# Kernel tuning notes

Hardware: AMD Instinct MI355X
Metric: run time of the kernel (lower is better)

Reference implementation:

```python
import jax, jax.numpy as jnp
import numpy as np

DIM = 1024
HEADS = 16
DIM_HEAD = 64
INNER = HEADS * DIM_HEAD  # 1024


def setup_inputs() -> dict:
    key = jax.random.key(0)
    k1, k2, k3, k4 = jax.random.split(key, 4)
    x = jax.random.normal(k1, (4, 2048, DIM), dtype=jnp.float32)
    # nn.Linear(dim, 3*inner, bias=False): weight (3*inner, dim); store transposed (dim, 3*inner)
    w_qkv = jax.random.normal(k2, (DIM, 3 * INNER), dtype=jnp.float32) * (DIM ** -0.5)
    # nn.Linear(inner, dim) with bias
    w_out = jax.random.normal(k3, (INNER, DIM), dtype=jnp.float32) * (INNER ** -0.5)
    b_out = jax.random.normal(k4, (DIM,), dtype=jnp.float32) * 0.01
    return {"x": x, "w_qkv": w_qkv, "w_out": w_out, "b_out": b_out}


def reference(x, w_qkv, w_out, b_out):
    b, n, _ = x.shape
    scale = DIM_HEAD ** -0.5
    qkv = x @ w_qkv  # [b, n, 3*inner]
    q, k, v = jnp.split(qkv, 3, axis=-1)
    # 'b n (h d) -> b h n d'
    def split_heads(t):
        return t.reshape(b, n, HEADS, DIM_HEAD).transpose(0, 2, 1, 3)
    q, k, v = split_heads(q), split_heads(k), split_heads(v)
    sim = jnp.einsum('bhid,bhjd->bhij', q, k) * scale  # [b, h, n, n]
    attn = jax.nn.softmax(sim, axis=-1)
    out = jnp.einsum('bhij,bhjd->bhid', attn, v)  # [b, h, n, d]
    out = out.transpose(0, 2, 1, 3).reshape(b, n, INNER)  # 'b h n d -> b n (h d)'
    return out @ w_out + b_out
```

## Files before the change

### kernel.cpp

```cpp
#include <hip/hip_runtime.h>
#include <hip/hip_bf16.h>

#define BATCH 4
#define SEQ   2048
#define DIM   1024
#define HEADS 16
#define DHEAD 64
#define INNER 1024
#define QKV_N 3072
#define MTOT  8192

typedef short bf16x8 __attribute__((ext_vector_type(8)));
typedef float f32x4  __attribute__((ext_vector_type(4)));
#define MFMA16(a,b,c) __builtin_amdgcn_mfma_f32_16x16x32_bf16((a),(b),(c),0,0,0)

#define QSCALE 0.1803368801111204f

static __device__ __forceinline__ unsigned fau(float f) { return __float_as_uint(f); }

static __device__ __forceinline__ uint2 pack_hi4(float4 v) {
    return make_uint2((fau(v.x) >> 16) | (fau(v.y) & 0xffff0000u),
                      (fau(v.z) >> 16) | (fau(v.w) & 0xffff0000u));
}
static __device__ __forceinline__ float4 resid4(float4 v) {
    float4 r;
    r.x = v.x - __uint_as_float(fau(v.x) & 0xffff0000u);
    r.y = v.y - __uint_as_float(fau(v.y) & 0xffff0000u);
    r.z = v.z - __uint_as_float(fau(v.z) & 0xffff0000u);
    r.w = v.w - __uint_as_float(fau(v.w) & 0xffff0000u);
    return r;
}
static __device__ __forceinline__ uint2 pack_lo4(float4 v) { return pack_hi4(resid4(v)); }

static __device__ __forceinline__ unsigned cvt_pk_bf16(float a, float b) {
    unsigned r;
    asm("v_cvt_pk_bf16_f32 %0, %1, %2" : "=v"(r) : "v"(a), "v"(b));
    return r;
}

__global__ __launch_bounds__(256) void pack_rows_hl(const float* __restrict__ src,
                                                    unsigned short* __restrict__ dst,
                                                    int Mtot, int K)
{
    const int m = blockIdx.x * 256 + threadIdx.x;
    const int t = blockIdx.y;
    const float* sp = src + (size_t)m * K + t * 32;
    unsigned short buf[64];
    #pragma unroll
    for (int i = 0; i < 32; i += 4) {
        const float4 v = *(const float4*)&sp[i];
        *(uint2*)&buf[i]      = pack_hi4(v);
        *(uint2*)&buf[32 + i] = pack_lo4(v);
    }
    unsigned short* dp = dst + ((size_t)t * Mtot + m) * 64;
    const int s7 = m & 7;
    #pragma unroll
    for (int G = 0; G < 8; ++G)
        *(bf16x8*)&dp[(G ^ s7) * 8] = *(bf16x8*)&buf[G * 8];
}

__global__ __launch_bounds__(256) void pack_cols_hl(const float* __restrict__ src,
                                                    unsigned short* __restrict__ dst,
                                                    int Ntot)
{
    const int n = blockIdx.x * 256 + threadIdx.x;
    const int t = blockIdx.y;
    float vals[32];
    #pragma unroll
    for (int i = 0; i < 32; ++i) vals[i] = src[(size_t)(t * 32 + i) * Ntot + n];
    unsigned short buf[64];
    #pragma unroll
    for (int i = 0; i < 32; i += 4) {
        const float4 v = make_float4(vals[i], vals[i + 1], vals[i + 2], vals[i + 3]);
        *(uint2*)&buf[i]      = pack_hi4(v);
        *(uint2*)&buf[32 + i] = pack_lo4(v);
    }
    unsigned short* dp = dst + ((size_t)t * Ntot + n) * 64;
    const int s7 = n & 7;
    #pragma unroll
    for (int G = 0; G < 8; ++G)
        *(bf16x8*)&dp[(G ^ s7) * 8] = *(bf16x8*)&buf[G * 8];
}

static __device__ __forceinline__ void gemm_core_pk(const unsigned short* __restrict__ Ap,
                                                    const unsigned short* __restrict__ Bp,
                                                    unsigned short* As,
                                                    unsigned short* Bs,
                                                    f32x4 (&acc)[4][4],
                                                    int Mtot, int Ntot, int NT,
                                                    int row0, int col0)
{
    const int tid  = threadIdx.x;
    const int lane = tid & 63;
    const int w    = tid >> 6;
    const int l15  = lane & 15;
    const int g    = lane >> 4;
    const int wr   = w >> 1, wc = w & 1;

    const unsigned short* aSrc = Ap + (size_t)row0 * 64 + tid * 8;
    const unsigned short* bSrc = Bp + (size_t)col0 * 64 + tid * 8;
    const size_t aStep = (size_t)Mtot * 64;
    const size_t bStep = (size_t)Ntot * 64;

    int aoff[4][2], boff[4][2];
    #pragma unroll
    for (int mt = 0; mt < 4; ++mt) {
        const int m = wr * 64 + mt * 16 + l15;
        const int sw = (m & 7) << 3;
        aoff[mt][0] = m * 64 + ((g * 8) ^ sw);
        aoff[mt][1] = m * 64 + ((32 + g * 8) ^ sw);
    }
    #pragma unroll
    for (int nt = 0; nt < 4; ++nt) {
        const int n = wc * 64 + nt * 16 + l15;
        const int sw = (n & 7) << 3;
        boff[nt][0] = n * 64 + ((g * 8) ^ sw);
        boff[nt][1] = n * 64 + ((32 + g * 8) ^ sw);
    }

    bf16x8 ar[4], br[4];
    #pragma unroll
    for (int p = 0; p < 4; ++p) {
        ar[p] = *(const bf16x8*)(aSrc + p * 2048);
        br[p] = *(const bf16x8*)(bSrc + p * 2048);
    }

    for (int t = 0; t < NT; ++t) {
        __syncthreads();
        #pragma unroll
        for (int p = 0; p < 4; ++p) {
            *(bf16x8*)&As[tid * 8 + p * 2048] = ar[p];
            *(bf16x8*)&Bs[tid * 8 + p * 2048] = br[p];
        }
        __syncthreads();
        if (t + 1 < NT) {
            const unsigned short* a2 = aSrc + (size_t)(t + 1) * aStep;
            const unsigned short* b2 = bSrc + (size_t)(t + 1) * bStep;
            #pragma unroll
            for (int p = 0; p < 4; ++p) {
                ar[p] = *(const bf16x8*)(a2 + p * 2048);
                br[p] = *(const bf16x8*)(b2 + p * 2048);
            }
        }
        bf16x8 ah[4], al[4], bh[4], bl[4];
        #pragma unroll
        for (int mt = 0; mt < 4; ++mt) {
            ah[mt] = *(const bf16x8*)&As[aoff[mt][0]];
            al[mt] = *(const bf16x8*)&As[aoff[mt][1]];
        }
        #pragma unroll
        for (int nt = 0; nt < 4; ++nt) {
            bh[nt] = *(const bf16x8*)&Bs[boff[nt][0]];
            bl[nt] = *(const bf16x8*)&Bs[boff[nt][1]];
        }
        #pragma unroll
        for (int mt = 0; mt < 4; ++mt)
            #pragma unroll
            for (int nt = 0; nt < 4; ++nt) {
                acc[mt][nt] = MFMA16(ah[mt], bh[nt], acc[mt][nt]);
                acc[mt][nt] = MFMA16(ah[mt], bl[nt], acc[mt][nt]);
                acc[mt][nt] = MFMA16(al[mt], bh[nt], acc[mt][nt]);
            }
    }
}

__global__ __launch_bounds__(256, 2) void gemm_out_pk(const unsigned short* __restrict__ Ap,
                                                      const unsigned short* __restrict__ Bp,
                                                      const float* __restrict__ bias,
                                                      float* __restrict__ C)
{
    __shared__ unsigned short As[128 * 64];
    __shared__ unsigned short Bs[128 * 64];

    const int tid  = threadIdx.x;
    const int lane = tid & 63;
    const int w    = tid >> 6;
    const int l15  = lane & 15;
    const int g    = lane >> 4;
    const int wr   = w >> 1, wc = w & 1;
    const int row0 = blockIdx.y * 128, col0 = blockIdx.x * 128;

    f32x4 acc[4][4] = {};
    gemm_core_pk(Ap, Bp, As, Bs, acc, MTOT, INNER, 32, row0, col0);

    #pragma unroll
    for (int nt = 0; nt < 4; ++nt) {
        const int c = col0 + wc * 64 + nt * 16 + l15;
        const float bv = bias[c];
        #pragma unroll
        for (int mt = 0; mt < 4; ++mt)
            #pragma unroll
            for (int r = 0; r < 4; ++r) {
                const int rr = row0 + wr * 64 + mt * 16 + g * 4 + r;
                C[(size_t)rr * INNER + c] = acc[mt][nt][r] + bv;
            }
    }
}

__global__ __launch_bounds__(256, 2) void gemm_qkv_pk(const unsigned short* __restrict__ Ap,
                                                      const unsigned short* __restrict__ Bp,
                                                      unsigned short* __restrict__ q_hl,
                                                      unsigned short* __restrict__ k_hl,
                                                      unsigned short* __restrict__ vt)
{
    __shared__ unsigned short As[128 * 64];
    __shared__ unsigned short Bs[128 * 64];

    const int tid  = threadIdx.x;
    const int lane = tid & 63;
    const int w    = tid >> 6;
    const int l15  = lane & 15;
    const int g    = lane >> 4;
    const int wr   = w >> 1, wc = w & 1;
    const int row0 = blockIdx.y * 128, col0 = blockIdx.x * 128;

    f32x4 acc[4][4] = {};
    gemm_core_pk(Ap, Bp, As, Bs, acc, MTOT, QKV_N, 32, row0, col0);

    if (col0 < 2 * INNER) {
        unsigned short* plane = (col0 < INNER) ? q_hl : k_hl;
        const float sc = (col0 < INNER) ? QSCALE : 1.0f;
        #pragma unroll
        for (int nt = 0; nt < 4; ++nt) {
            const int c  = col0 + wc * 64 + nt * 16 + l15;
            const int cc = c & (INNER - 1);
            const int hd = (cc >> 6) * 128 + (cc & 63);
            #pragma unroll
            for (int mt = 0; mt < 4; ++mt)
                #pragma unroll
                for (int r = 0; r < 4; ++r) {
                    const int rr = row0 + wr * 64 + mt * 16 + g * 4 + r;
                    const float v = acc[mt][nt][r] * sc;
                    const unsigned u = fau(v);
                    const float res = v - __uint_as_float(u & 0xffff0000u);
                    unsigned short* dp = plane + (size_t)rr * 2048 + hd;
                    dp[0]  = (unsigned short)(u >> 16);
                    dp[64] = (unsigned short)(fau(res) >> 16);
                }
        }
    } else {
        #pragma unroll
        for (int nt = 0; nt < 4; ++nt) {
            const int f = col0 + wc * 64 + nt * 16 + l15 - 2 * INNER;
            #pragma unroll
            for (int mt = 0; mt < 4; ++mt) {
                const int rr0 = row0 + wr * 64 + mt * 16 + g * 4;
                const int bb  = rr0 >> 11;
                const int n   = rr0 & (SEQ - 1);
                const int pn  = (n & ~31) | ((n & 12) << 1) | ((n & 16) >> 2);
                const uint2 pk = make_uint2(
                    cvt_pk_bf16(acc[mt][nt][0], acc[mt][nt][1]),
                    cvt_pk_bf16(acc[mt][nt][2], acc[mt][nt][3]));
                *(uint2*)&vt[((size_t)bb * INNER + f) * SEQ + pn] = pk;
            }
        }
    }
}

__global__ __launch_bounds__(256, 2) void attn_mfma(const unsigned short* __restrict__ q_hl,
                                                    const unsigned short* __restrict__ k_hl,
                                                    const unsigned short* __restrict__ vt,
                                                    unsigned short* __restrict__ ao_hl)
{
    __shared__ unsigned short Ks[64 * 128];
    __shared__ unsigned short Vs[64 * 64];

    const int tid  = threadIdx.x;
    const int lane = tid & 63;
    const int w    = tid >> 6;
    const int l15  = lane & 15;
    const int g    = lane >> 4;
    const int qb = blockIdx.x, h = blockIdx.y, b = blockIdx.z;
    const int q0 = qb * 256 + w * 64;

    bf16x8 qh[4][2], ql[4][2];
    #pragma unroll
    for (int qs = 0; qs < 4; ++qs) {
        const unsigned short* qp =
            q_hl + (size_t)(b * SEQ + q0 + qs * 16 + l15) * 2048 + h * 128;
        #pragma unroll
        for (int kk = 0; kk < 2; ++kk) {
            qh[qs][kk] = *(const bf16x8*)&qp[kk * 32 + g * 8];
            ql[qs][kk] = *(const bf16x8*)&qp[64 + kk * 32 + g * 8];
        }
    }

    f32x4 o[4][4] = {};
    float m_run[4] = {-1e30f, -1e30f, -1e30f, -1e30f};
    float l_run[4] = {0.f, 0.f, 0.f, 0.f};

    const int kj   = tid >> 4;
    const int ko8  = (tid & 15) * 8;
    const int kdst = kj * 128 + (ko8 ^ (kj << 3));
    const unsigned short* ksrc =
        k_hl + ((size_t)(b * SEQ + kj)) * 2048 + h * 128 + ko8;

    const int vd   = tid >> 3;
    const int vu8  = (tid & 7) * 8;
    const int vdst = vd * 64 + (vu8 ^ ((vd & 7) << 3));
    const unsigned short* vsrc =
        vt + ((size_t)(b * HEADS + h) * 64 + vd) * SEQ + vu8;

    const int krow = l15 * 128;
    int koff[2][2];
    #pragma unroll
    for (int kk = 0; kk < 2; ++kk) {
        koff[kk][0] = (kk * 32 + g * 8) ^ (l15 * 8);
        koff[kk][1] = (64 + kk * 32 + g * 8) ^ (l15 * 8);
    }
    const int vrow = l15 * 64;
    const int voff[2] = { (g * 8) ^ ((l15 & 7) * 8), (32 + g * 8) ^ ((l15 & 7) * 8) };

    for (int kv = 0; kv < SEQ / 64; ++kv) {
        const int j0 = kv * 64;
        __syncthreads();
        #pragma unroll
        for (int p = 0; p < 4; ++p)
            *(bf16x8*)&Ks[p * 2048 + kdst] =
                *(const bf16x8*)&ksrc[(size_t)(j0 + p * 16) * 2048];
        #pragma unroll
        for (int p = 0; p < 2; ++p)
            *(bf16x8*)&Vs[p * 2048 + vdst] =
                *(const bf16x8*)&vsrc[(size_t)p * 32 * SEQ + j0];
        __syncthreads();

        f32x4 s[4][4] = {};
        #pragma unroll
        for (int jt = 0; jt < 4; ++jt) {
            #pragma unroll
            for (int kk = 0; kk < 2; ++kk) {
                const bf16x8 khf = *(const bf16x8*)&Ks[jt * 2048 + krow + koff[kk][0]];
                const bf16x8 klf = *(const bf16x8*)&Ks[jt * 2048 + krow + koff[kk][1]];
                #pragma unroll
                for (int qs = 0; qs < 4; ++qs) {
                    s[qs][jt] = MFMA16(khf, qh[qs][kk], s[qs][jt]);
                    s[qs][jt] = MFMA16(khf, ql[qs][kk], s[qs][jt]);
                    s[qs][jt] = MFMA16(klf, qh[qs][kk], s[qs][jt]);
                }
            }
        }

        bf16x8 pav[4][2];
        #pragma unroll
        for (int qs = 0; qs < 4; ++qs) {
            float mx = -1e30f;
            #pragma unroll
            for (int jt = 0; jt < 4; ++jt)
                #pragma unroll
                for (int r = 0; r < 4; ++r) mx = fmaxf(mx, s[qs][jt][r]);
            mx = fmaxf(mx, __shfl_xor(mx, 16));
            mx = fmaxf(mx, __shfl_xor(mx, 32));
            if (!__all(mx - m_run[qs] <= 8.f)) {
                const float mnew = fmaxf(m_run[qs], mx);
                const float corr = __builtin_amdgcn_exp2f(m_run[qs] - mnew);
                m_run[qs] = mnew;
                l_run[qs] *= corr;
                const float cr0 = __shfl(corr, g * 4 + 0);
                const float cr1 = __shfl(corr, g * 4 + 1);
                const float cr2 = __shfl(corr, g * 4 + 2);
                const float cr3 = __shfl(corr, g * 4 + 3);
                #pragma unroll
                for (int nt = 0; nt < 4; ++nt) {
                    o[qs][nt][0] *= cr0; o[qs][nt][1] *= cr1;
                    o[qs][nt][2] *= cr2; o[qs][nt][3] *= cr3;
                }
            }
            float sm = 0.f;
            #pragma unroll
            for (int jt = 0; jt < 4; ++jt)
                #pragma unroll
                for (int r = 0; r < 4; ++r) {
                    const float e = __builtin_amdgcn_exp2f(s[qs][jt][r] - m_run[qs]);
                    s[qs][jt][r] = e; sm += e;
                }
            sm += __shfl_xor(sm, 16);
            sm += __shfl_xor(sm, 32);
            l_run[qs] += sm;

            #pragma unroll
            for (int t = 0; t < 2; ++t) {
                union { uint2 u[2]; bf16x8 v; } P;
                P.u[0] = make_uint2(cvt_pk_bf16(s[qs][2 * t][0],     s[qs][2 * t][1]),
                                    cvt_pk_bf16(s[qs][2 * t][2],     s[qs][2 * t][3]));
                P.u[1] = make_uint2(cvt_pk_bf16(s[qs][2 * t + 1][0], s[qs][2 * t + 1][1]),
                                    cvt_pk_bf16(s[qs][2 * t + 1][2], s[qs][2 * t + 1][3]));
                pav[qs][t] = P.v;
            }
        }

        #pragma unroll
        for (int t = 0; t < 2; ++t)
            #pragma unroll
            for (int nt = 0; nt < 4; ++nt) {
                const bf16x8 vb = *(const bf16x8*)&Vs[nt * 1024 + vrow + voff[t]];
                #pragma unroll
                for (int qs = 0; qs < 4; ++qs)
                    o[qs][nt] = MFMA16(pav[qs][t], vb, o[qs][nt]);
            }
    }

    #pragma unroll
    for (int qs = 0; qs < 4; ++qs) {
        const float il = 1.f / l_run[qs];
        const float nr0 = __shfl(il, g * 4 + 0);
        const float nr1 = __shfl(il, g * 4 + 1);
        const float nr2 = __shfl(il, g * 4 + 2);
        const float nr3 = __shfl(il, g * 4 + 3);
        const float nr[4] = {nr0, nr1, nr2, nr3};
        #pragma unroll
        for (int nt = 0; nt < 4; ++nt) {
            const int k  = h * DHEAD + nt * 16 + l15;
            const int t  = k >> 5;
            const int kk = k & 31;
            const int G  = kk >> 3;
            const int e  = kk & 7;
            #pragma unroll
            for (int r = 0; r < 4; ++r) {
                const int M  = b * SEQ + q0 + qs * 16 + g * 4 + r;
                const int s7 = M & 7;
                unsigned short* dp = ao_hl + ((size_t)t * MTOT + M) * 64;
                const float v = o[qs][nt][r] * nr[r];
                const unsigned u = fau(v);
                const float res = v - __uint_as_float(u & 0xffff0000u);
                dp[((G ^ s7) << 3) + e]       = (unsigned short)(u >> 16);
                dp[(((G + 4) ^ s7) << 3) + e] = (unsigned short)(fau(res) >> 16);
            }
        }
    }
}

extern "C" void kernel_launch(void* const* d_in, const int* in_sizes, int n_in,
                              void* d_out, int out_size, void* d_ws, size_t ws_size,
                              hipStream_t stream)
{
    const float* x     = (const float*)d_in[0];
    const float* w_qkv = (const float*)d_in[1];
    const float* w_out = (const float*)d_in[2];
    const float* b_out = (const float*)d_in[3];
    float* out = (float*)d_out;

    unsigned short* q_hl  = (unsigned short*)d_ws;
    unsigned short* k_hl  = q_hl  + (size_t)MTOT * 2048;
    unsigned short* vt    = k_hl  + (size_t)MTOT * 2048;
    unsigned short* xa_hl = vt    + (size_t)BATCH * INNER * SEQ;
    unsigned short* wq_hl = xa_hl + (size_t)32 * MTOT * 64;
    unsigned short* wo_hl = wq_hl + (size_t)32 * QKV_N * 64;

    pack_rows_hl<<<dim3(MTOT / 256, 32), 256, 0, stream>>>(x, xa_hl, MTOT, DIM);
    pack_cols_hl<<<dim3(QKV_N / 256, 32), 256, 0, stream>>>(w_qkv, wq_hl, QKV_N);
    pack_cols_hl<<<dim3(INNER / 256, 32), 256, 0, stream>>>(w_out, wo_hl, INNER);

    gemm_qkv_pk<<<dim3(QKV_N / 128, MTOT / 128), 256, 0, stream>>>(
        xa_hl, wq_hl, q_hl, k_hl, vt);

    attn_mfma<<<dim3(SEQ / 256, HEADS, BATCH), 256, 0, stream>>>(
        q_hl, k_hl, vt, xa_hl);

    gemm_out_pk<<<dim3(INNER / 128, MTOT / 128), 256, 0, stream>>>(
        xa_hl, wo_hl, b_out, out);
}
```

Baseline: 362.6 us.

## Double-buffer LDS in GEMM and attention kernels, add MFMA priority hints

```diff
diff --git a/kernel.cpp b/kernel.cpp
--- a/kernel.cpp
+++ b/kernel.cpp
@@ -17,6 +17,9 @@
 #define QSCALE 0.1803368801111204f
 
 static __device__ __forceinline__ unsigned fau(float f) { return __float_as_uint(f); }
+static __device__ __forceinline__ float max3f(float a, float b, float c) {
+    return fmaxf(fmaxf(a, b), c);
+}
 
 static __device__ __forceinline__ uint2 pack_hi4(float4 v) {
     return make_uint2((fau(v.x) >> 16) | (fau(v.y) & 0xffff0000u),
@@ -125,12 +128,12 @@
         br[p] = *(const bf16x8*)(bSrc + p * 2048);
     }
 
+    int cur = 0;
     for (int t = 0; t < NT; ++t) {
-        __syncthreads();
         #pragma unroll
         for (int p = 0; p < 4; ++p) {
-            *(bf16x8*)&As[tid * 8 + p * 2048] = ar[p];
-            *(bf16x8*)&Bs[tid * 8 + p * 2048] = br[p];
+            *(bf16x8*)&As[cur * 8192 + tid * 8 + p * 2048] = ar[p];
+            *(bf16x8*)&Bs[cur * 8192 + tid * 8 + p * 2048] = br[p];
         }
         __syncthreads();
         if (t + 1 < NT) {
@@ -145,13 +148,13 @@
         bf16x8 ah[4], al[4], bh[4], bl[4];
         #pragma unroll
         for (int mt = 0; mt < 4; ++mt) {
-            ah[mt] = *(const bf16x8*)&As[aoff[mt][0]];
-            al[mt] = *(const bf16x8*)&As[aoff[mt][1]];
+            ah[mt] = *(const bf16x8*)&As[cur * 8192 + aoff[mt][0]];
+            al[mt] = *(const bf16x8*)&As[cur * 8192 + aoff[mt][1]];
         }
         #pragma unroll
         for (int nt = 0; nt < 4; ++nt) {
-            bh[nt] = *(const bf16x8*)&Bs[boff[nt][0]];
-            bl[nt] = *(const bf16x8*)&Bs[boff[nt][1]];
+            bh[nt] = *(const bf16x8*)&Bs[cur * 8192 + boff[nt][0]];
+            bl[nt] = *(const bf16x8*)&Bs[cur * 8192 + boff[nt][1]];
         }
         #pragma unroll
         for (int mt = 0; mt < 4; ++mt)
@@ -161,6 +164,7 @@
                 acc[mt][nt] = MFMA16(ah[mt], bl[nt], acc[mt][nt]);
                 acc[mt][nt] = MFMA16(al[mt], bh[nt], acc[mt][nt]);
             }
+        cur ^= 1;
     }
 }
 
@@ -169,8 +173,8 @@
                                                       const float* __restrict__ bias,
                                                       float* __restrict__ C)
 {
-    __shared__ unsigned short As[128 * 64];
-    __shared__ unsigned short Bs[128 * 64];
+    __shared__ unsigned short As[2 * 128 * 64];
+    __shared__ unsigned short Bs[2 * 128 * 64];
 
     const int tid  = threadIdx.x;
     const int lane = tid & 63;
@@ -203,8 +207,8 @@
                                                       unsigned short* __restrict__ k_hl,
                                                       unsigned short* __restrict__ vt)
 {
-    __shared__ unsigned short As[128 * 64];
-    __shared__ unsigned short Bs[128 * 64];
+    __shared__ unsigned short As[2 * 128 * 64];
+    __shared__ unsigned short Bs[2 * 128 * 64];
 
     const int tid  = threadIdx.x;
     const int lane = tid & 63;
@@ -262,15 +266,15 @@
                                                     const unsigned short* __restrict__ vt,
                                                     unsigned short* __restrict__ ao_hl)
 {
-    __shared__ unsigned short Ks[64 * 128];
-    __shared__ unsigned short Vs[64 * 64];
+    __shared__ unsigned short Ks[2 * 64 * 128];
+    __shared__ unsigned short Vs[2 * 64 * 64];
 
     const int tid  = threadIdx.x;
     const int lane = tid & 63;
     const int w    = tid >> 6;
     const int l15  = lane & 15;
     const int g    = lane >> 4;
-    const int qb = blockIdx.x, h = blockIdx.y, b = blockIdx.z;
+    const int h  = blockIdx.x, qb = blockIdx.y, b = blockIdx.z;
     const int q0 = qb * 256 + w * 64;
 
     bf16x8 qh[4][2], ql[4][2];
@@ -311,26 +315,42 @@
     const int vrow = l15 * 64;
     const int voff[2] = { (g * 8) ^ ((l15 & 7) * 8), (32 + g * 8) ^ ((l15 & 7) * 8) };
 
+    bf16x8 kr[4], vr[2];
+    #pragma unroll
+    for (int p = 0; p < 4; ++p)
+        kr[p] = *(const bf16x8*)&ksrc[(size_t)(p * 16) * 2048];
+    #pragma unroll
+    for (int p = 0; p < 2; ++p)
+        vr[p] = *(const bf16x8*)&vsrc[(size_t)p * 32 * SEQ];
+
+    int cur = 0;
     for (int kv = 0; kv < SEQ / 64; ++kv) {
-        const int j0 = kv * 64;
+        const int kb = cur * 8192, vb = cur * 4096;
+        #pragma unroll
+        for (int p = 0; p < 4; ++p)
+            *(bf16x8*)&Ks[kb + p * 2048 + kdst] = kr[p];
+        #pragma unroll
+        for (int p = 0; p < 2; ++p)
+            *(bf16x8*)&Vs[vb + p * 2048 + vdst] = vr[p];
         __syncthreads();
-        #pragma unroll
-        for (int p = 0; p < 4; ++p)
-            *(bf16x8*)&Ks[p * 2048 + kdst] =
-                *(const bf16x8*)&ksrc[(size_t)(j0 + p * 16) * 2048];
-        #pragma unroll
-        for (int p = 0; p < 2; ++p)
-            *(bf16x8*)&Vs[p * 2048 + vdst] =
-                *(const bf16x8*)&vsrc[(size_t)p * 32 * SEQ + j0];
-        __syncthreads();
+        if (kv + 1 < SEQ / 64) {
+            const int j0n = (kv + 1) * 64;
+            #pragma unroll
+            for (int p = 0; p < 4; ++p)
+                kr[p] = *(const bf16x8*)&ksrc[(size_t)(j0n + p * 16) * 2048];
+            #pragma unroll
+            for (int p = 0; p < 2; ++p)
+                vr[p] = *(const bf16x8*)&vsrc[(size_t)p * 32 * SEQ + j0n];
+        }
 
         f32x4 s[4][4] = {};
+        __builtin_amdgcn_s_setprio(1);
         #pragma unroll
         for (int jt = 0; jt < 4; ++jt) {
             #pragma unroll
             for (int kk = 0; kk < 2; ++kk) {
-                const bf16x8 khf = *(const bf16x8*)&Ks[jt * 2048 + krow + koff[kk][0]];
-                const bf16x8 klf = *(const bf16x8*)&Ks[jt * 2048 + krow + koff[kk][1]];
+                const bf16x8 khf = *(const bf16x8*)&Ks[kb + jt * 2048 + krow + koff[kk][0]];
+                const bf16x8 klf = *(const bf16x8*)&Ks[kb + jt * 2048 + krow + koff[kk][1]];
                 #pragma unroll
                 for (int qs = 0; qs < 4; ++qs) {
                     s[qs][jt] = MFMA16(khf, qh[qs][kk], s[qs][jt]);
@@ -339,15 +359,20 @@
                 }
             }
         }
+        __builtin_amdgcn_s_setprio(0);
 
         bf16x8 pav[4][2];
         #pragma unroll
         for (int qs = 0; qs < 4; ++qs) {
-            float mx = -1e30f;
-            #pragma unroll
-            for (int jt = 0; jt < 4; ++jt)
-                #pragma unroll
-                for (int r = 0; r < 4; ++r) mx = fmaxf(mx, s[qs][jt][r]);
+            const f32x4* sq = s[qs];
+            float mx = max3f(sq[0][0], sq[0][1], sq[0][2]);
+            mx = max3f(mx, sq[0][3], sq[1][0]);
+            mx = max3f(mx, sq[1][1], sq[1][2]);
+            mx = max3f(mx, sq[1][3], sq[2][0]);
+            mx = max3f(mx, sq[2][1], sq[2][2]);
+            mx = max3f(mx, sq[2][3], sq[3][0]);
+            mx = max3f(mx, sq[3][1], sq[3][2]);
+            mx = fmaxf(mx, sq[3][3]);
             mx = fmaxf(mx, __shfl_xor(mx, 16));
             mx = fmaxf(mx, __shfl_xor(mx, 32));
             if (!__all(mx - m_run[qs] <= 8.f)) {
@@ -388,15 +413,18 @@
             }
         }
 
+        __builtin_amdgcn_s_setprio(1);
         #pragma unroll
         for (int t = 0; t < 2; ++t)
             #pragma unroll
             for (int nt = 0; nt < 4; ++nt) {
-                const bf16x8 vb = *(const bf16x8*)&Vs[nt * 1024 + vrow + voff[t]];
+                const bf16x8 vbv = *(const bf16x8*)&Vs[vb + nt * 1024 + vrow + voff[t]];
                 #pragma unroll
                 for (int qs = 0; qs < 4; ++qs)
-                    o[qs][nt] = MFMA16(pav[qs][t], vb, o[qs][nt]);
-            }
+                    o[qs][nt] = MFMA16(pav[qs][t], vbv, o[qs][nt]);
+            }
+        __builtin_amdgcn_s_setprio(0);
+        cur ^= 1;
     }
 
     #pragma unroll
@@ -453,7 +481,7 @@
     gemm_qkv_pk<<<dim3(QKV_N / 128, MTOT / 128), 256, 0, stream>>>(
         xa_hl, wq_hl, q_hl, k_hl, vt);
 
-    attn_mfma<<<dim3(SEQ / 256, HEADS, BATCH), 256, 0, stream>>>(
+    attn_mfma<<<dim3(HEADS, SEQ / 256, BATCH), 256, 0, stream>>>(
         q_hl, k_hl, vt, xa_hl);
 
     gemm_out_pk<<<dim3(INNER / 128, MTOT / 128), 256, 0, stream>>>(
```

Result: faster. 350.1 us (-3.5%).
